# Optimization experiments

Measured on AMD Instinct MI355X. Metric: run time of the kernel, lower is better.

## Reference

```python
import jax, jax.numpy as jnp
import numpy as np
from jax import lax

D_MODEL = 64
D_STATE = 128
D_INNER = 128  # d_model * expand_factor; must equal D_STATE for the original code to broadcast
BATCH = 4
SEQ = 1024
LN_EPS = 1e-5


def setup_inputs() -> dict:
    key = jax.random.key(0)
    ks = jax.random.split(key, 12)
    s = 0.05
    return {
        "x": jax.random.normal(ks[0], (BATCH, SEQ, D_MODEL), jnp.float32),
        "W_in": jax.random.normal(ks[1], (2 * D_INNER, D_MODEL), jnp.float32) * s,
        "W_delta": jax.random.normal(ks[2], (D_INNER, D_MODEL), jnp.float32) * s,
        "b_delta": jax.random.normal(ks[3], (D_INNER,), jnp.float32) * s,
        "W_B": jax.random.normal(ks[4], (D_STATE, D_MODEL), jnp.float32) * s,
        "b_B": jax.random.normal(ks[5], (D_STATE,), jnp.float32) * s,
        "W_C": jax.random.normal(ks[6], (D_STATE, D_MODEL), jnp.float32) * s,
        "b_C": jax.random.normal(ks[7], (D_STATE,), jnp.float32) * s,
        "A": jax.random.normal(ks[8], (D_INNER, D_STATE), jnp.float32) * 0.01,
        "W_out": jax.random.normal(ks[9], (D_MODEL, D_INNER), jnp.float32) * s,
        "ln_w": jnp.ones((D_MODEL,), jnp.float32),
        "ln_b": jnp.zeros((D_MODEL,), jnp.float32),
    }


def _layer_norm(x, w, b):
    mu = x.mean(-1, keepdims=True)
    var = ((x - mu) ** 2).mean(-1, keepdims=True)
    return (x - mu) * lax.rsqrt(var + LN_EPS) * w + b


def reference(x, W_in, W_delta, b_delta, W_B, b_B, W_C, b_C, A, W_out, ln_w, ln_b):
    # projections
    xp = jnp.einsum('bld,ed->ble', x, W_in)            # (B, L, 2*d_inner)
    x_ssm, gate = xp[..., :D_INNER], xp[..., D_INNER:]
    delta = jax.nn.softplus(jnp.einsum('bld,id->bli', x, W_delta) + b_delta)  # (B, L, d_inner)
    Bm = jnp.einsum('bld,sd->bls', x, W_B) + b_B        # (B, L, d_state)
    Cm = jnp.einsum('bld,sd->bls', x, W_C) + b_C        # (B, L, d_state)

    # A_discrete.mean(dim=1): mean over d_inner of exp(delta * A)
    Abar = jnp.exp(delta[..., :, None] * A).mean(axis=2)  # (B, L, d_state)
    x_pool = x_ssm.mean(axis=-1)                          # (B, L) mean over d_inner
    Bx = Bm * x_pool[..., None]                           # (B, L, d_state)

    def step(h, inp):
        a_t, bx_t, c_t = inp                              # each (B, d_state)
        h = a_t * h + bx_t
        y = (c_t * h).sum(axis=-1)                        # (B,)
        return h, y

    h0 = jnp.zeros((x.shape[0], D_STATE), x.dtype)
    _, ys = lax.scan(step, h0,
                     (jnp.swapaxes(Abar, 0, 1), jnp.swapaxes(Bx, 0, 1), jnp.swapaxes(Cm, 0, 1)))
    y = jnp.swapaxes(ys, 0, 1)[..., None]                 # (B, L, 1) -> broadcast over d_inner

    y = y * jax.nn.silu(gate)                             # (B, L, d_inner)
    out = jnp.einsum('bli,di->bld', y, W_out)             # (B, L, d_model)
    return _layer_norm(out + x, ln_w, ln_b)
```

## Files before the change

### kernel.cpp

```cpp
#include <hip/hip_runtime.h>
#include <math.h>

#define NB   4
#define SL   1024
#define NTOK (NB*SL)
#define DM   64
#define DI   128
#define DSt  128
#define SEGLEN 8
#define NSEG (SL/SEGLEN)
#define NSEG_ALL (NB*NSEG)

#define OFF_GATE   0
#define OFF_DELTA  (OFF_GATE  + NTOK*DI)
#define OFF_BM     (OFF_DELTA + NTOK*DI)
#define OFF_CM     (OFF_BM    + NTOK*DSt)
#define OFF_XPOOL  (OFF_CM    + NTOK*DSt)
#define OFF_ABAR   (OFF_XPOOL + NTOK)
#define OFF_HEND   (OFF_ABAR  + NTOK*DSt)
#define OFF_P      (OFF_HEND  + NSEG_ALL*DSt)
#define OFF_W4     (OFF_P     + NSEG_ALL*DSt)

#define PROJ_TOK 16
#define PROJ_TG  (NTOK/PROJ_TOK)

static __device__ __forceinline__ float wave64_sum(float v) {
#pragma unroll
    for (int m = 32; m >= 1; m >>= 1) v += __shfl_xor(v, m, 64);
    return v;
}

static __device__ __forceinline__ float fast_exp2(float x) {
    float r;
    asm("v_exp_f32 %0, %1" : "=v"(r) : "v"(x));
    return r;
}

static __device__ __forceinline__ float softplus_f(float x) {
    return fmaxf(x, 0.f) + __logf(1.f + __expf(-fabsf(x)));
}

static __device__ __forceinline__ void pin4(float4& v) {
    asm volatile("" : "+v"(v.x), "+v"(v.y), "+v"(v.z), "+v"(v.w));
}

#if __has_builtin(__builtin_amdgcn_global_load_lds)
#define HAVE_GLL 1
static __device__ __forceinline__ void gload_lds16(const float4* g, float4* l) {
    __builtin_amdgcn_global_load_lds(
        (const __attribute__((address_space(1))) void*)g,
        (__attribute__((address_space(3))) void*)l,
        16, 0, 0);
}
#else
#define HAVE_GLL 0
#endif

__global__ __launch_bounds__(256, 2) void k_proj(
    const float* __restrict__ x, const float* __restrict__ W_in,
    const float* __restrict__ W_delta, const float* __restrict__ b_delta,
    const float* __restrict__ W_B, const float* __restrict__ b_B,
    const float* __restrict__ W_C, const float* __restrict__ b_C,
    const float* __restrict__ W_out, float* __restrict__ ws)
{
    __shared__ float4 Wl[DI*16];
    const int tid = threadIdx.x;

    if (blockIdx.x == 4*PROJ_TG) {
        const float4* Wg = (const float4*)W_out;
        float4* W4 = (float4*)(ws + OFF_W4);
#pragma unroll
        for (int j = 0; j < 8; ++j) {
            const int f = tid + j*256;
            const int d = f >> 5, q = f & 31;
            W4[q*64 + d] = Wg[f];
        }
        return;
    }

    const int l   = tid & 63;
    const int w   = tid >> 6;
    const int cat = blockIdx.x >> 8;
    const int tg  = blockIdx.x & 255;
    const int tok0 = tg * PROJ_TOK;

    const float* Wbase; const float* bias; float* dst;
    if      (cat == 0) { Wbase = W_in + DI*DM; bias = nullptr; dst = ws + OFF_GATE;  }
    else if (cat == 1) { Wbase = W_delta;      bias = b_delta; dst = ws + OFF_DELTA; }
    else if (cat == 2) { Wbase = W_B;          bias = b_B;     dst = ws + OFF_BM;    }
    else               { Wbase = W_C;          bias = b_C;     dst = ws + OFF_CM;    }

    {
        const float4* Wg = (const float4*)Wbase;
#if HAVE_GLL
#pragma unroll
        for (int j = 0; j < 8; ++j) {
            const int f   = tid + j*256;
            const int row = f >> 4, kk = f & 15;
            const int src = row*16 + (kk ^ (row & 15));
            gload_lds16(Wg + src, Wl + f);
        }
#else
#pragma unroll
        for (int j = 0; j < 8; ++j) {
            const int f = tid + j*256;
            const int row = f >> 4, k = f & 15;
            Wl[row*16 + (k ^ (row & 15))] = Wg[f];
        }
#endif
    }
    __syncthreads();

    float4 w0[16], w1[16];
#pragma unroll
    for (int k = 0; k < 16; ++k) {
        w0[k] = Wl[l*16      + (k ^ (l & 15))];
        w1[k] = Wl[(l+64)*16 + (k ^ (l & 15))];
    }
#pragma unroll
    for (int k = 0; k < 16; ++k) { pin4(w0[k]); pin4(w1[k]); }

    float bias0 = 0.f, bias1 = 0.f;
    if (bias) { bias0 = bias[l]; bias1 = bias[l+64]; }

#pragma unroll
    for (int it = 0; it < PROJ_TOK/4; ++it) {
        const int tlu = __builtin_amdgcn_readfirstlane(it*4 + w);
        const float4* xt = (const float4*)(x + (tok0 + tlu)*DM);
        float a0=0.f,a1=0.f,a2=0.f,a3=0.f, c0=0.f,c1=0.f,c2=0.f,c3=0.f;
#pragma unroll
        for (int k = 0; k < 16; ++k) {
            const float4 xv = xt[k];
            a0 = fmaf(w0[k].x, xv.x, a0);
            a1 = fmaf(w0[k].y, xv.y, a1);
            a2 = fmaf(w0[k].z, xv.z, a2);
            a3 = fmaf(w0[k].w, xv.w, a3);
            c0 = fmaf(w1[k].x, xv.x, c0);
            c1 = fmaf(w1[k].y, xv.y, c1);
            c2 = fmaf(w1[k].z, xv.z, c2);
            c3 = fmaf(w1[k].w, xv.w, c3);
        }
        float ra = (a0+a1) + (a2+a3) + bias0;
        float rb = (c0+c1) + (c2+c3) + bias1;
        if (cat == 1) { ra = softplus_f(ra); rb = softplus_f(rb); }
        const int tok = tok0 + tlu;
        dst[tok*128 + l]      = ra;
        dst[tok*128 + 64 + l] = rb;
    }

    if (cat == 0) {
        float wp = 0.f;
#pragma unroll 8
        for (int i = 0; i < DI; ++i) wp += W_in[i*DM + l];
        wp *= (1.0f/DI);
#pragma unroll
        for (int it = 0; it < PROJ_TOK/4; ++it) {
            const int tl = it*4 + w;
            float v = x[(tok0 + tl)*DM + l] * wp;
            v = wave64_sum(v);
            if (l == 0) ws[OFF_XPOOL + tok0 + tl] = v;
        }
    }
}

__global__ __launch_bounds__(256) void k_abar_scan1(const float* __restrict__ A,
                                                    float* __restrict__ ws)
{
    __shared__ float psum[4][SEGLEN][64];
    __shared__ float abL[SEGLEN][64];
    const int tid  = threadIdx.x;
    const int lane = tid & 63;
    const int igrp = tid >> 6;
    const int g    = blockIdx.x >> 1;
    const int sh   = blockIdx.x & 1;
    const int s    = sh*64 + lane;
    const int t0   = g * SEGLEN;

    float areg[32];
#pragma unroll
    for (int i = 0; i < 32; ++i)
        areg[i] = A[(igrp*32 + i)*DSt + s] * 1.44269504f;

    const float* delta = ws + OFF_DELTA;
    float*       Abar  = ws + OFF_ABAR;

#pragma unroll
    for (int t = 0; t < SEGLEN; ++t) {
        const float* dv = delta + (t0 + t)*DI + igrp*32;
        float a0=0.f,a1=0.f,a2=0.f,a3=0.f;
#pragma unroll
        for (int q = 0; q < 8; ++q) {
            const float4 d4 = *(const float4*)(dv + 4*q);
            a0 += fast_exp2(d4.x * areg[4*q    ]);
            a1 += fast_exp2(d4.y * areg[4*q + 1]);
            a2 += fast_exp2(d4.z * areg[4*q + 2]);
            a3 += fast_exp2(d4.w * areg[4*q + 3]);
        }
        psum[igrp][t][lane] = (a0+a1) + (a2+a3);
    }
    __syncthreads();

#pragma unroll
    for (int it = tid; it < SEGLEN*64; it += 256) {
        const int t = it >> 6, l2 = it & 63;
        float v = (psum[0][t][l2] + psum[1][t][l2])
                + (psum[2][t][l2] + psum[3][t][l2]);
        v *= (1.0f/DI);
        abL[t][l2] = v;
        Abar[(t0 + t)*DSt + sh*64 + l2] = v;
    }
    __syncthreads();

    if (tid < 64) {
        const float* Bm    = ws + OFF_BM;
        const float* xpool = ws + OFF_XPOOL;
        float bx[SEGLEN];
#pragma unroll
        for (int t = 0; t < SEGLEN; ++t)
            bx[t] = Bm[(t0 + t)*DSt + s] * xpool[t0 + t];
        float h = 0.f, pr = 1.f;
#pragma unroll
        for (int t = 0; t < SEGLEN; ++t) {
            const float a = abL[t][lane];
            h = fmaf(a, h, bx[t]);
            pr *= a;
        }
        ws[OFF_HEND + g*DSt + s] = h;
        ws[OFF_P    + g*DSt + s] = pr;
    }
}

__global__ __launch_bounds__(256) void k_tail(
    const float* __restrict__ x, const float* __restrict__ ln_w,
    const float* __restrict__ ln_b, const float* __restrict__ ws,
    float* __restrict__ out)
{
    __shared__ float prod[SEGLEN][132];
    __shared__ float y_lds[SEGLEN];
    __shared__ float vbuf[4][DI];

    const int tid = threadIdx.x;
    const int b   = blockIdx.x >> 7;
    const int seg = blockIdx.x & 127;
    const int t0  = b*SL + seg*SEGLEN;
    const int d   = tid & 63;
    const int wv  = tid >> 6;

    const float* gate = ws + OFF_GATE;
    float g0[2], g1[2], xres[2];
#pragma unroll
    for (int jt = 0; jt < 2; ++jt) {
        const int tok = t0 + wv*2 + jt;
        g0[jt]   = gate[tok*DI + d];
        g1[jt]   = gate[tok*DI + 64 + d];
        xres[jt] = x[tok*DM + d];
    }
    const float lw = ln_w[d], lb = ln_b[d];

    if (tid < 128) {
        const int s = tid;
        const float* Abar  = ws + OFF_ABAR;
        const float* Bm    = ws + OFF_BM;
        const float* Cm    = ws + OFF_CM;
        const float* xpool = ws + OFF_XPOOL;
        const float* hend  = ws + OFF_HEND;
        const float* P     = ws + OFF_P;

        float aA[SEGLEN], aB[SEGLEN], aC[SEGLEN];
#pragma unroll
        for (int t = 0; t < SEGLEN; ++t) {
            aA[t] = Abar[(t0 + t)*DSt + s];
            aB[t] = Bm[(t0 + t)*DSt + s] * xpool[t0 + t];
            aC[t] = Cm[(t0 + t)*DSt + s];
        }
        float h = 0.f;
#pragma unroll 8
        for (int j = 0; j < seg; ++j) {
            const int idx = (b*NSEG + j)*DSt + s;
            h = fmaf(P[idx], h, hend[idx]);
        }
#pragma unroll
        for (int t = 0; t < SEGLEN; ++t) {
            h = fmaf(aA[t], h, aB[t]);
            prod[t][s] = aC[t] * h;
        }
    }
    __syncthreads();

    if (tid < 128) {
        const int t = tid >> 4, r = tid & 15;
        float4 u0 = *(const float4*)(&prod[t][r*8]);
        float4 u1 = *(const float4*)(&prod[t][r*8 + 4]);
        float acc = ((u0.x+u0.y) + (u0.z+u0.w)) + ((u1.x+u1.y) + (u1.z+u1.w));
#pragma unroll
        for (int m = 1; m <= 8; m <<= 1) acc += __shfl_xor(acc, m, 64);
        if (r == 0) y_lds[t] = acc;
    }
    __syncthreads();

    const float4* W4 = (const float4*)(ws + OFF_W4);
#pragma unroll
    for (int jt = 0; jt < 2; ++jt) {
        const int tl  = wv*2 + jt;
        const int tok = t0 + tl;
        const float yt = y_lds[tl];
        vbuf[wv][d]      = yt * (g0[jt] / (1.f + __expf(-g0[jt])));
        vbuf[wv][64 + d] = yt * (g1[jt] / (1.f + __expf(-g1[jt])));

        float ac0 = 0.f, ac1 = 0.f, ac2 = 0.f, ac3 = 0.f;
#pragma unroll 8
        for (int q = 0; q < 32; ++q) {
            const float4 wv4 = W4[q*64 + d];
            const float4 vv  = *(const float4*)(&vbuf[wv][q*4]);
            ac0 = fmaf(wv4.x, vv.x, ac0);
            ac1 = fmaf(wv4.y, vv.y, ac1);
            ac2 = fmaf(wv4.z, vv.z, ac2);
            ac3 = fmaf(wv4.w, vv.w, ac3);
        }
        const float z  = (ac0+ac1) + (ac2+ac3) + xres[jt];
        const float s1 = wave64_sum(z);
        const float s2 = wave64_sum(z*z);
        const float mu  = s1 * (1.f/64.f);
        const float var = s2 * (1.f/64.f) - mu*mu;
        out[tok*DM + d] = (z - mu) * rsqrtf(var + 1e-5f) * lw + lb;
    }
}

extern "C" void kernel_launch(void* const* d_in, const int* in_sizes, int n_in,
                              void* d_out, int out_size, void* d_ws, size_t ws_size,
                              hipStream_t stream) {
    const float* x       = (const float*)d_in[0];
    const float* W_in    = (const float*)d_in[1];
    const float* W_delta = (const float*)d_in[2];
    const float* b_delta = (const float*)d_in[3];
    const float* W_B     = (const float*)d_in[4];
    const float* b_B     = (const float*)d_in[5];
    const float* W_C     = (const float*)d_in[6];
    const float* b_C     = (const float*)d_in[7];
    const float* A       = (const float*)d_in[8];
    const float* W_out   = (const float*)d_in[9];
    const float* ln_w    = (const float*)d_in[10];
    const float* ln_b    = (const float*)d_in[11];
    float* out = (float*)d_out;
    float* ws  = (float*)d_ws;

    hipLaunchKernelGGL(k_proj, dim3(4*PROJ_TG + 1), dim3(256), 0, stream,
                       x, W_in, W_delta, b_delta, W_B, b_B, W_C, b_C, W_out, ws);
    hipLaunchKernelGGL(k_abar_scan1, dim3(2*NSEG_ALL), dim3(256), 0, stream, A, ws);
    hipLaunchKernelGGL(k_tail,       dim3(NSEG_ALL),   dim3(256), 0, stream,
                       x, ln_w, ln_b, ws, out);
}
```

Measured before the change: 46.00 us.

## Split output projection over inner dim across waves with register-held W_out slices

The tail kernel's output projection is restructured so each wave owns a quarter of the inner dimension. It keeps its W_out slice in registers, loaded up front, and computes partial sums for all 8 tokens, which are then reduced through shared memory. Previously each wave re-read the full W_out from global memory once for each of its two tokens. The gate loads are also coalesced across the block and the SiLU-gated vector is built for all tokens at once. This adds LDS usage and two extra barriers, and raises register pressure.

```diff
diff --git a/kernel.cpp b/kernel.cpp
--- a/kernel.cpp
+++ b/kernel.cpp
@@ -237,7 +237,8 @@
 {
     __shared__ float prod[SEGLEN][132];
     __shared__ float y_lds[SEGLEN];
-    __shared__ float vbuf[4][DI];
+    __shared__ float vall[SEGLEN][DI];
+    __shared__ float psum[4][SEGLEN][64];
 
     const int tid = threadIdx.x;
     const int b   = blockIdx.x >> 7;
@@ -247,14 +248,22 @@
     const int wv  = tid >> 6;
 
     const float* gate = ws + OFF_GATE;
-    float g0[2], g1[2], xres[2];
-#pragma unroll
-    for (int jt = 0; jt < 2; ++jt) {
-        const int tok = t0 + wv*2 + jt;
-        g0[jt]   = gate[tok*DI + d];
-        g1[jt]   = gate[tok*DI + 64 + d];
-        xres[jt] = x[tok*DM + d];
-    }
+    const float4* W4  = (const float4*)(ws + OFF_W4);
+    float gv[4];
+#pragma unroll
+    for (int j = 0; j < 4; ++j) {
+        const int idx = j*256 + tid;
+        const int tl = idx >> 7, dd = idx & 127;
+        gv[j] = gate[(t0 + tl)*DI + dd];
+    }
+    float4 wq[8];
+#pragma unroll
+    for (int j = 0; j < 8; ++j)
+        wq[j] = W4[(wv*8 + j)*64 + d];
+    float xres[2];
+#pragma unroll
+    for (int jt = 0; jt < 2; ++jt)
+        xres[jt] = x[(t0 + wv*2 + jt)*DM + d];
     const float lw = ln_w[d], lb = ln_b[d];
 
     if (tid < 128) {
@@ -298,26 +307,40 @@
     }
     __syncthreads();
 
-    const float4* W4 = (const float4*)(ws + OFF_W4);
+#pragma unroll
+    for (int j = 0; j < 4; ++j) {
+        const int idx = j*256 + tid;
+        const int tl = idx >> 7, dd = idx & 127;
+        const float g = gv[j];
+        vall[tl][dd] = y_lds[tl] * (g / (1.f + __expf(-g)));
+    }
+    __syncthreads();
+
+    float ac[8];
+#pragma unroll
+    for (int t = 0; t < 8; ++t) ac[t] = 0.f;
+#pragma unroll
+    for (int j = 0; j < 8; ++j) {
+        const float4 w4 = wq[j];
+#pragma unroll
+        for (int t = 0; t < 8; ++t) {
+            const float4 v = *(const float4*)(&vall[t][(wv*8 + j)*4]);
+            ac[t] = fmaf(w4.x, v.x, ac[t]);
+            ac[t] = fmaf(w4.y, v.y, ac[t]);
+            ac[t] = fmaf(w4.z, v.z, ac[t]);
+            ac[t] = fmaf(w4.w, v.w, ac[t]);
+        }
+    }
+#pragma unroll
+    for (int t = 0; t < 8; ++t) psum[wv][t][d] = ac[t];
+    __syncthreads();
+
 #pragma unroll
     for (int jt = 0; jt < 2; ++jt) {
         const int tl  = wv*2 + jt;
         const int tok = t0 + tl;
-        const float yt = y_lds[tl];
-        vbuf[wv][d]      = yt * (g0[jt] / (1.f + __expf(-g0[jt])));
-        vbuf[wv][64 + d] = yt * (g1[jt] / (1.f + __expf(-g1[jt])));
-
-        float ac0 = 0.f, ac1 = 0.f, ac2 = 0.f, ac3 = 0.f;
-#pragma unroll 8
-        for (int q = 0; q < 32; ++q) {
-            const float4 wv4 = W4[q*64 + d];
-            const float4 vv  = *(const float4*)(&vbuf[wv][q*4]);
-            ac0 = fmaf(wv4.x, vv.x, ac0);
-            ac1 = fmaf(wv4.y, vv.y, ac1);
-            ac2 = fmaf(wv4.z, vv.z, ac2);
-            ac3 = fmaf(wv4.w, vv.w, ac3);
-        }
-        const float z  = (ac0+ac1) + (ac2+ac3) + xres[jt];
+        const float z = ((psum[0][tl][d] + psum[1][tl][d])
+                       + (psum[2][tl][d] + psum[3][tl][d])) + xres[jt];
         const float s1 = wave64_sum(z);
         const float s2 = wave64_sum(z*z);
         const float mu  = s1 * (1.f/64.f);
```

Measured after the change: 43.83 us, median of 2. -4.7%, faster.
